# Performance work log

Measured on AMD Instinct MI355X. Metric: run time of the kernel, lower is better.

The kernel has to match this reference:

```python
import jax, jax.numpy as jnp
import numpy as np

BITS = 8
BOUND = 2.0 ** (BITS - 1) - 1.0  # 127, symmetric int8 bound
EPS = 1e-6


def fake_quant(x, scale):
    """Symmetric fake quantization with straight-through estimator."""
    q = jnp.clip(jnp.round(x * scale), -BOUND, BOUND) / scale
    return x + jax.lax.stop_gradient(q - x)


def dense_aqt(x, w, b, mask):
    """AQT-style quantized dense: per-tensor input scale (masked stats),
    per-output-channel weight scale, int8-range fake quant, float GEMM.
    x: [N, Cin], w: [Cin, Cout], b: [Cout], mask: [N, 1]."""
    x_max = jnp.max(jnp.abs(x * mask))                       # masked per-tensor stat
    sx = BOUND / jnp.maximum(x_max, EPS)
    w_max = jnp.max(jnp.abs(w), axis=0, keepdims=True)        # [1, Cout]
    sw = BOUND / jnp.maximum(w_max, EPS)
    xq = fake_quant(x, sx)
    wq = fake_quant(w, sw)
    return jnp.matmul(xq, wq) + b


def setup_inputs() -> dict:
    key = jax.random.key(0)
    k1, k2, k3 = jax.random.split(key, 3)
    B, S, C, H = 4, 2048, 1024, 4096
    inputs = jax.random.normal(k1, (B, S, C), dtype=jnp.float32)
    padding_mask = jnp.ones((B, S, 1), dtype=jnp.float32)
    W1 = jax.random.normal(k2, (C, H), dtype=jnp.float32) * (1.0 / np.sqrt(C))
    b1 = jnp.zeros((H,), dtype=jnp.float32)
    W2 = jax.random.normal(k3, (H, C), dtype=jnp.float32) * (1.0 / np.sqrt(H))
    b2 = jnp.zeros((C,), dtype=jnp.float32)
    return {"inputs": inputs, "padding_mask": padding_mask,
            "W1": W1, "b1": b1, "W2": W2, "b2": b2}


def reference(inputs, padding_mask, W1, b1, W2, b2):
    B, S, C = inputs.shape
    x = inputs.reshape(B * S, C)
    m = padding_mask.reshape(B * S, 1)
    h = jax.nn.relu(dense_aqt(x, W1, b1, m))   # dropout is no-op (deterministic)
    out = dense_aqt(h, W2, b2, m)              # dropout is no-op (deterministic)
    return out.reshape(B, S, C)
```

## Files before the change

### kernel.cpp

```cpp
#include <hip/hip_runtime.h>
#include <hip/hip_fp16.h>
#include <stdint.h>


#define EPSQ 1e-6f
typedef int v4i __attribute__((ext_vector_type(4)));
typedef int v16i __attribute__((ext_vector_type(16)));

__device__ __forceinline__ void async16(const int8_t* g, int8_t* l) {
  __builtin_amdgcn_global_load_lds(
      (const __attribute__((address_space(1))) void*)g,
      (__attribute__((address_space(3))) void*)l, 16, 0, 0);
}
__device__ __forceinline__ unsigned short f2h(float f) {
  __half h = __float2half(f);
  return *(unsigned short*)&h;
}
__device__ __forceinline__ float4 max4(float4 m, float4 v) {
  m.x = fmaxf(m.x, fabsf(v.x)); m.y = fmaxf(m.y, fabsf(v.y));
  m.z = fmaxf(m.z, fabsf(v.z)); m.w = fmaxf(m.w, fabsf(v.w));
  return m;
}
__device__ __forceinline__ unsigned qmb(float x, float s) {
  return __float_as_uint(fmaf(x, s, 12582912.0f)) & 0xffu;
}
__device__ __forceinline__ unsigned q4f(float4 f, float s) {
  return qmb(f.x, s) | (qmb(f.y, s) << 8) | (qmb(f.z, s) << 16) |
         (__float_as_uint(fmaf(f.w, s, 12582912.0f)) << 24);
}
__device__ __forceinline__ unsigned q4h(unsigned ua, unsigned ub,
                                        __half2 s2, __half2 m2) {
  __half2 ha = __hfma2(*(__half2*)&ua, s2, m2);
  __half2 hb = __hfma2(*(__half2*)&ub, s2, m2);
  unsigned va = *(unsigned*)&ha, vb = *(unsigned*)&hb;
#if __has_builtin(__builtin_amdgcn_perm)
  return __builtin_amdgcn_perm(vb, va, 0x06040200u);
#else
  return (va & 0xffu) | ((va >> 8) & 0xff00u) |
         ((vb & 0xffu) << 16) | (((vb >> 8) & 0xff00u) << 16);
#endif
}

__global__ __launch_bounds__(256) void k_stats(
    const float* __restrict__ x, const float* __restrict__ mask,
    const float* __restrict__ W1, const float* __restrict__ W2,
    float* __restrict__ pmaxX, float* __restrict__ pcm1, float* __restrict__ pcm2) {
  const int bx = blockIdx.x, tid = threadIdx.x;
  if (bx < 64) {
    const int sp = bx & 15, cg = bx >> 4;
    const int col = cg * 1024 + tid * 4;
    float4 m = {0.f, 0.f, 0.f, 0.f};
#pragma unroll 8
    for (int r = 0; r < 64; ++r)
      m = max4(m, *(const float4*)(W1 + (size_t)(sp * 64 + r) * 4096 + col));
    *(float4*)(pcm1 + sp * 4096 + col) = m;
  } else if (bx < 128) {
    const int sp = bx - 64;
    const int col = tid * 4;
    float4 m = {0.f, 0.f, 0.f, 0.f};
#pragma unroll 8
    for (int r = 0; r < 64; ++r)
      m = max4(m, *(const float4*)(W2 + (size_t)(sp * 64 + r) * 1024 + col));
    *(float4*)(pcm2 + sp * 1024 + col) = m;
  } else {
    __shared__ float red[4];
    const int b = bx - 128;
    float lmax = 0.f;
    for (int c = b * 256 + tid; c < 1048576; c += 262144) {
      size_t idx = (size_t)c * 8;
      float mk = fabsf(mask[idx >> 10]);
      float4 m4 = {0.f, 0.f, 0.f, 0.f};
      m4 = max4(m4, *(const float4*)(x + idx));
      m4 = max4(m4, *(const float4*)(x + idx + 4));
      lmax = fmaxf(lmax, fmaxf(fmaxf(m4.x, m4.y), fmaxf(m4.z, m4.w)) * mk);
    }
    for (int s = 32; s; s >>= 1) lmax = fmaxf(lmax, __shfl_down(lmax, s));
    if ((tid & 63) == 0) red[tid >> 6] = lmax;
    __syncthreads();
    if (tid == 0)
      pmaxX[b] = fmaxf(fmaxf(red[0], red[1]), fmaxf(red[2], red[3]));
  }
}

__global__ __launch_bounds__(256) void k_quant(
    const float* __restrict__ x, const float* __restrict__ W1, const float* __restrict__ W2,
    const float* __restrict__ pmaxX, const float* __restrict__ pcm1, const float* __restrict__ pcm2,
    int8_t* __restrict__ qx, int8_t* __restrict__ qw1, int8_t* __restrict__ qw2,
    float* __restrict__ cm1, float* __restrict__ cm2, float* __restrict__ scG) {
  const int bx = blockIdx.x, tid = threadIdx.x;
  if (bx < 2048) {
    __shared__ float red[4];
    float v = fmaxf(fmaxf(pmaxX[tid], pmaxX[tid + 256]),
                    fmaxf(pmaxX[tid + 512], pmaxX[tid + 768]));
    for (int s = 32; s; s >>= 1) v = fmaxf(v, __shfl_down(v, s));
    if ((tid & 63) == 0) red[tid >> 6] = v;
    __syncthreads();
    const float xmax = fmaxf(fmaxf(red[0], red[1]), fmaxf(red[2], red[3]));
    if (bx == 0 && tid == 0) scG[0] = xmax;
    const float s = 127.0f / fmaxf(xmax, EPSQ);
    const int wave = tid >> 6, lane = tid & 63;
    const int f = bx * 4 + wave;
    const int r = (f >> 5) * 32 + (lane & 31);
    const int k = (f & 31) * 32 + (lane >> 5) * 16;
    const float4* src = (const float4*)(x + (size_t)r * 1024 + k);
    uint4 o;
    o.x = q4f(src[0], s); o.y = q4f(src[1], s);
    o.z = q4f(src[2], s); o.w = q4f(src[3], s);
    *(uint4*)(qx + (size_t)f * 1024 + lane * 16) = o;
  } else if (bx < 2304) {
    int id = (bx - 2048) * 256 + tid;
    int n4 = id & 1023, kc = id >> 10;
    const int col = n4 * 4;
    float4 cm = {0.f, 0.f, 0.f, 0.f};
#pragma unroll
    for (int sp = 0; sp < 16; ++sp) {
      float4 p = *(const float4*)(pcm1 + sp * 4096 + col);
      cm.x = fmaxf(cm.x, p.x); cm.y = fmaxf(cm.y, p.y);
      cm.z = fmaxf(cm.z, p.z); cm.w = fmaxf(cm.w, p.w);
    }
    if (kc == 0) *(float4*)(cm1 + col) = cm;
    const float s0 = 127.0f / fmaxf(cm.x, EPSQ), s1 = 127.0f / fmaxf(cm.y, EPSQ);
    const float s2 = 127.0f / fmaxf(cm.z, EPSQ), s3 = 127.0f / fmaxf(cm.w, EPSQ);
    union { int8_t p[16]; uint4 v; } u0, u1, u2, u3;
#pragma unroll
    for (int j = 0; j < 16; ++j) {
      float4 f = *(const float4*)(W1 + (size_t)(kc * 16 + j) * 4096 + col);
      u0.p[j] = (int8_t)qmb(f.x, s0); u1.p[j] = (int8_t)qmb(f.y, s1);
      u2.p[j] = (int8_t)qmb(f.z, s2); u3.p[j] = (int8_t)qmb(f.w, s3);
    }
    int8_t* base = qw1 + ((size_t)(col >> 5) * 32 + (kc >> 1)) * 1024 +
                   (kc & 1) * 512 + (col & 31) * 16;
    *(uint4*)(base) = u0.v;      *(uint4*)(base + 16) = u1.v;
    *(uint4*)(base + 32) = u2.v; *(uint4*)(base + 48) = u3.v;
  } else {
    int id = (bx - 2304) * 256 + tid;
    int n4 = id & 255, kc = id >> 8;
    const int col = n4 * 4;
    float4 cm = {0.f, 0.f, 0.f, 0.f};
#pragma unroll
    for (int sp = 0; sp < 64; ++sp) {
      float4 p = *(const float4*)(pcm2 + sp * 1024 + col);
      cm.x = fmaxf(cm.x, p.x); cm.y = fmaxf(cm.y, p.y);
      cm.z = fmaxf(cm.z, p.z); cm.w = fmaxf(cm.w, p.w);
    }
    if (kc == 0) *(float4*)(cm2 + col) = cm;
    const float s0 = 127.0f / fmaxf(cm.x, EPSQ), s1 = 127.0f / fmaxf(cm.y, EPSQ);
    const float s2 = 127.0f / fmaxf(cm.z, EPSQ), s3 = 127.0f / fmaxf(cm.w, EPSQ);
    union { int8_t p[16]; uint4 v; } u0, u1, u2, u3;
#pragma unroll
    for (int j = 0; j < 16; ++j) {
      float4 f = *(const float4*)(W2 + (size_t)(kc * 16 + j) * 1024 + col);
      u0.p[j] = (int8_t)qmb(f.x, s0); u1.p[j] = (int8_t)qmb(f.y, s1);
      u2.p[j] = (int8_t)qmb(f.z, s2); u3.p[j] = (int8_t)qmb(f.w, s3);
    }
    int8_t* base = qw2 + ((size_t)(col >> 5) * 128 + (kc >> 1)) * 1024 +
                   (kc & 1) * 512 + (col & 31) * 16;
    *(uint4*)(base) = u0.v;      *(uint4*)(base + 16) = u1.v;
    *(uint4*)(base + 32) = u2.v; *(uint4*)(base + 48) = u3.v;
  }
}

__global__ __launch_bounds__(512, 6) void gemm1(
    const int8_t* __restrict__ A, const int8_t* __restrict__ Bt,
    const float* __restrict__ sxp, const float* __restrict__ cmax,
    const float* __restrict__ bias, const float* __restrict__ mask,
    unsigned short* __restrict__ hfrag, float* __restrict__ pmaxH) {
  constexpr int NST = 16;
  __shared__ __align__(16) int8_t smem[3 * 16384];
  const int tid = threadIdx.x;
  const int wave = tid >> 6, lane = tid & 63;

  const int bid = blockIdx.x;
  const int xcd = bid & 7, sl = bid >> 3;
  const int m0 = ((xcd & 3) * 16 + (sl & 15)) * 128;
  const int n0 = ((xcd >> 2) * 16 + (sl >> 4)) * 128;
  const int wm = (wave & 1) * 64, wn = (wave >> 1) * 32;

  v16i acc[2] = {};

  const int skc = wave >> 2, sfr = wave & 3;
  const int8_t* gA = A  + ((size_t)((m0 >> 5) + sfr) * 32 + skc) * 1024 + lane * 16;
  const int8_t* gB = Bt + ((size_t)((n0 >> 5) + sfr) * 32 + skc) * 1024 + lane * 16;
  const int soff = (skc * 4 + sfr) * 1024 + lane * 16;

  async16(gA, smem + soff);
  async16(gB, smem + 8192 + soff);
  async16(gA + 2048, smem + 16384 + soff);
  async16(gB + 2048, smem + 16384 + 8192 + soff);
  asm volatile("s_waitcnt vmcnt(2)" ::: "memory");
  __builtin_amdgcn_s_barrier();
  __builtin_amdgcn_sched_barrier(0);

  const int mI = (wave & 1) * 2, nb = wave >> 1;
#pragma unroll
  for (int kb = 0; kb < NST; ++kb) {
    const int co = (kb % 3) * 16384;
    if (kb + 2 < NST) {
      const int po = ((kb + 2) % 3) * 16384;
      async16(gA + (kb + 2) * 2048, smem + po + soff);
      async16(gB + (kb + 2) * 2048, smem + po + 8192 + soff);
    }
    __builtin_amdgcn_sched_barrier(0);
#pragma unroll
    for (int kc = 0; kc < 2; ++kc) {
      v4i af0 = *(const v4i*)(smem + co + (kc * 4 + mI) * 1024 + lane * 16);
      v4i af1 = *(const v4i*)(smem + co + (kc * 4 + mI + 1) * 1024 + lane * 16);
      v4i bf  = *(const v4i*)(smem + co + 8192 + (kc * 4 + nb) * 1024 + lane * 16);
      acc[0] = __builtin_amdgcn_mfma_i32_32x32x32_i8(af0, bf, acc[0], 0, 0, 0);
      acc[1] = __builtin_amdgcn_mfma_i32_32x32x32_i8(af1, bf, acc[1], 0, 0, 0);
    }
    if (kb + 1 < NST) {
      asm volatile("s_waitcnt lgkmcnt(0)" ::: "memory");
      if (kb + 2 < NST)
        asm volatile("s_waitcnt vmcnt(2)" ::: "memory");
      else
        asm volatile("s_waitcnt vmcnt(0)" ::: "memory");
      __builtin_amdgcn_s_barrier();
      __builtin_amdgcn_sched_barrier(0);
    }
  }

  const float asc = fmaxf(sxp[0], EPSQ) * (1.0f / 127.0f);
  const int cl = lane & 31;
  const int rbase = 4 * (lane >> 5);
  const int col = n0 + wn + cl;
  const float bsc = fmaxf(cmax[col], EPSQ) * (1.0f / 127.0f) * asc;
  const float bv = bias[col];
  const int hwoff = (cl >> 4) * 512 + (cl & 15);
  const size_t kblk = (size_t)(n0 + wn) >> 5;
  float lmax = 0.f;
#pragma unroll
  for (int mt = 0; mt < 2; ++mt) {
    const size_t rowblk = (size_t)((m0 + wm + mt * 32) >> 5);
    unsigned short* hb = hfrag + (rowblk * 128 + kblk) * 1024 + hwoff;
    const int rowbase = m0 + wm + mt * 32;
#pragma unroll
    for (int g = 0; g < 4; ++g)
#pragma unroll
      for (int r2 = 0; r2 < 4; ++r2) {
        const int rloc = g * 8 + r2 + rbase;
        const float mk = fabsf(mask[rowbase + rloc]);
        float v = (float)acc[mt][g * 4 + r2] * bsc + bv;
        v = fmaxf(v, 0.f);
        hb[rloc * 16] = f2h(v);
        lmax = fmaxf(lmax, v * mk);
      }
  }
  for (int s = 32; s; s >>= 1) lmax = fmaxf(lmax, __shfl_down(lmax, s));
  __syncthreads();
  float* redf = (float*)smem;
  if (lane == 0) redf[wave] = lmax;
  __syncthreads();
  if (tid == 0) {
    float r = redf[0];
#pragma unroll
    for (int j = 1; j < 8; ++j) r = fmaxf(r, redf[j]);
    pmaxH[bid] = r;
  }
}

__global__ __launch_bounds__(512, 4) void gemm2(
    const unsigned short* __restrict__ hfrag, const int8_t* __restrict__ Bt,
    const float* __restrict__ pmaxH, const float* __restrict__ cmax,
    const float* __restrict__ bias, float* __restrict__ out) {
  constexpr int KF = 2, Kf = 128;
  __shared__ __align__(16) int8_t smem[32768];
  int8_t* const lsA = smem;
  int8_t* const lsB = smem + 16384;
  const int tid = threadIdx.x;
  const int wave = tid >> 6, lane = tid & 63;

  float* red = (float*)smem;
  float v = 0.f;
#pragma unroll
  for (int j = 0; j < 4; ++j) v = fmaxf(v, pmaxH[tid + 512 * j]);
  for (int s = 32; s; s >>= 1) v = fmaxf(v, __shfl_down(v, s));
  if (lane == 0) red[wave] = v;
  __syncthreads();
  float hmax = red[0];
#pragma unroll
  for (int j = 1; j < 8; ++j) hmax = fmaxf(hmax, red[j]);
  __syncthreads();
  const float asc = fmaxf(hmax, EPSQ) * (1.0f / 127.0f);
  const __half sh = __float2half_rn(127.0f / fmaxf(hmax, EPSQ));
  const __half2 s2 = __halves2half2(sh, sh);
  const __half mh = __float2half_rn(1536.0f);
  const __half2 m2 = __halves2half2(mh, mh);

  const int bid = blockIdx.x;
  const int xcd = bid & 7, slot = bid >> 3;
  const int m0 = ((xcd << 3) + (slot >> 3)) * 128;
  const int n0 = (slot & 7) * 128;
  const int wm = (wave & 1) * 64, wn = (wave >> 1) * 32;

  v16i acc[2] = {};

  const int skc = wave >> 2, sfr = wave & 3;
  const uint4* hA = (const uint4*)hfrag;
  const size_t aIdx = ((size_t)((m0 >> 5) + sfr) * Kf + skc) * 128 + lane * 2;
  const int8_t* gB = Bt + ((size_t)((n0 >> 5) + sfr) * Kf + skc) * 1024 + lane * 16;
  int8_t* const dA = lsA + (skc * 4 + sfr) * 1024 + lane * 16;
  int8_t* const dB = lsB + (skc * 4 + sfr) * 1024 + lane * 16;

  const int nsteps = 4096 / (32 * KF);
  const int mI = (wave & 1) * 2, nb = wave >> 1;

  uint4 rA0 = {0, 0, 0, 0}, rB0 = {0, 0, 0, 0};
  uint4 rA1 = {0, 0, 0, 0}, rB1 = {0, 0, 0, 0};

  {
    uint4 a = hA[aIdx], b = hA[aIdx + 1];
    async16(gB, dB);
    __builtin_amdgcn_sched_barrier(0);
    rA1 = hA[aIdx + (size_t)(KF * 128)];
    rB1 = hA[aIdx + (size_t)(KF * 128) + 1];
    uint4 o;
    o.x = q4h(a.x, a.y, s2, m2); o.y = q4h(a.z, a.w, s2, m2);
    o.z = q4h(b.x, b.y, s2, m2); o.w = q4h(b.z, b.w, s2, m2);
    *(uint4*)dA = o;
  }
  asm volatile("s_waitcnt lgkmcnt(0)" ::: "memory");
  asm volatile("s_waitcnt vmcnt(2)" ::: "memory");
  __builtin_amdgcn_s_barrier();
  __builtin_amdgcn_sched_barrier(0);

#pragma unroll 2
  for (int kb = 0; kb < nsteps; ++kb) {
    const int cur = kb & 1;
    const int co = cur * 8192, po = co ^ 8192;
    const bool more = (kb + 1 < nsteps);
    const bool deep = (kb + 2 < nsteps);
    if (more) {
      async16(gB + (size_t)(kb + 1) * (KF * 1024), dB + po);
      __builtin_amdgcn_sched_barrier(0);
      if (deep) {
        const size_t ai = aIdx + (size_t)(kb + 2) * (KF * 128);
        if (cur) { rA1 = hA[ai]; rB1 = hA[ai + 1]; }
        else     { rA0 = hA[ai]; rB0 = hA[ai + 1]; }
      }
    }
#pragma unroll
    for (int kc = 0; kc < KF; ++kc) {
      v4i af0 = *(const v4i*)(lsA + co + (kc * 4 + mI) * 1024 + lane * 16);
      v4i af1 = *(const v4i*)(lsA + co + (kc * 4 + mI + 1) * 1024 + lane * 16);
      v4i bf  = *(const v4i*)(lsB + co + (kc * 4 + nb) * 1024 + lane * 16);
      acc[0] = __builtin_amdgcn_mfma_i32_32x32x32_i8(af0, bf, acc[0], 0, 0, 0);
      acc[1] = __builtin_amdgcn_mfma_i32_32x32x32_i8(af1, bf, acc[1], 0, 0, 0);
    }
    if (more) {
      const uint4 pa = cur ? rA0 : rA1;
      const uint4 pb = cur ? rB0 : rB1;
      uint4 o;
      o.x = q4h(pa.x, pa.y, s2, m2); o.y = q4h(pa.z, pa.w, s2, m2);
      o.z = q4h(pb.x, pb.y, s2, m2); o.w = q4h(pb.z, pb.w, s2, m2);
      *(uint4*)(dA + po) = o;
      asm volatile("s_waitcnt lgkmcnt(0)" ::: "memory");
      if (deep) asm volatile("s_waitcnt vmcnt(2)" ::: "memory");
      else      asm volatile("s_waitcnt vmcnt(0)" ::: "memory");
      __builtin_amdgcn_s_barrier();
      __builtin_amdgcn_sched_barrier(0);
    }
  }

  const int cl = lane & 31;
  const int rbase = 4 * (lane >> 5);
  const int col = n0 + wn + cl;
  const float bsc = fmaxf(cmax[col], EPSQ) * (1.0f / 127.0f) * asc;
  const float bv = bias[col];
#pragma unroll
  for (int mt = 0; mt < 2; ++mt)
#pragma unroll
    for (int g = 0; g < 4; ++g)
#pragma unroll
      for (int r2 = 0; r2 < 4; ++r2) {
        const int row = m0 + wm + mt * 32 + g * 8 + r2 + rbase;
        out[(size_t)row * 1024 + col] = (float)acc[mt][g * 4 + r2] * bsc + bv;
      }
}

extern "C" void kernel_launch(void* const* d_in, const int* in_sizes, int n_in,
                              void* d_out, int out_size, void* d_ws, size_t ws_size,
                              hipStream_t stream) {
  const float* x  = (const float*)d_in[0];
  const float* mk = (const float*)d_in[1];
  const float* W1 = (const float*)d_in[2];
  const float* b1 = (const float*)d_in[3];
  const float* W2 = (const float*)d_in[4];
  const float* b2 = (const float*)d_in[5];
  float* out = (float*)d_out;

  float* scG   = (float*)d_ws;
  float* pmaxX = scG + 8;
  float* pmaxH = pmaxX + 1024;
  float* pcm1  = pmaxH + 2048;
  float* pcm2  = pcm1 + 65536;
  float* cm1   = pcm2 + 65536;
  float* cm2   = cm1 + 4096;
  int8_t* qx  = (int8_t*)(cm2 + 1024);
  int8_t* qw1 = qx  + (size_t)8192 * 1024;
  int8_t* qw2 = qw1 + (size_t)4096 * 1024;
  unsigned short* h = (unsigned short*)(qw2 + (size_t)1024 * 4096);

  k_stats<<<1152, 256, 0, stream>>>(x, mk, W1, W2, pmaxX, pcm1, pcm2);
  k_quant<<<2560, 256, 0, stream>>>(x, W1, W2, pmaxX, pcm1, pcm2,
                                    qx, qw1, qw2, cm1, cm2, scG);
  gemm1<<<2048, 512, 0, stream>>>(qx, qw1, scG, cm1, b1, mk, h, pmaxH);
  gemm2<<<512, 512, 0, stream>>>(h, qw2, pmaxH, cm2, b2, out);
}
```

Measured before the change: 223.1 us.

## Give each wave a 2x2 MFMA tile and enlarge gemm1 block tile

gemm1 now computes a 256x128 tile per block (1024 blocks), with each wave holding a 2x2 grid of 32x32 accumulators, so every A and B fragment read from LDS feeds two MFMAs. gemm2 drops to 256 threads per block, with each wave also computing a 2x2 accumulator tile and loading two k-fragments of A and B per thread. The aim is more MFMA work per LDS read and per global load. The cost is more registers and LDS per block, lower occupancy (launch bounds 4 and 2), and fewer waves to hide latency.

```diff
diff --git a/kernel.cpp b/kernel.cpp
--- a/kernel.cpp
+++ b/kernel.cpp
@@ -160,59 +160,66 @@
   }
 }
 
-__global__ __launch_bounds__(512, 6) void gemm1(
+__global__ __launch_bounds__(512, 4) void gemm1(
     const int8_t* __restrict__ A, const int8_t* __restrict__ Bt,
     const float* __restrict__ sxp, const float* __restrict__ cmax,
     const float* __restrict__ bias, const float* __restrict__ mask,
     unsigned short* __restrict__ hfrag, float* __restrict__ pmaxH) {
   constexpr int NST = 16;
-  __shared__ __align__(16) int8_t smem[3 * 16384];
+  constexpr int BUF = 24576;
+  __shared__ __align__(16) int8_t smem[3 * BUF];
   const int tid = threadIdx.x;
   const int wave = tid >> 6, lane = tid & 63;
 
   const int bid = blockIdx.x;
   const int xcd = bid & 7, sl = bid >> 3;
-  const int m0 = ((xcd & 3) * 16 + (sl & 15)) * 128;
-  const int n0 = ((xcd >> 2) * 16 + (sl >> 4)) * 128;
-  const int wm = (wave & 1) * 64, wn = (wave >> 1) * 32;
-
-  v16i acc[2] = {};
-
-  const int skc = wave >> 2, sfr = wave & 3;
-  const int8_t* gA = A  + ((size_t)((m0 >> 5) + sfr) * 32 + skc) * 1024 + lane * 16;
-  const int8_t* gB = Bt + ((size_t)((n0 >> 5) + sfr) * 32 + skc) * 1024 + lane * 16;
-  const int soff = (skc * 4 + sfr) * 1024 + lane * 16;
-
-  async16(gA, smem + soff);
-  async16(gB, smem + 8192 + soff);
-  async16(gA + 2048, smem + 16384 + soff);
-  async16(gB + 2048, smem + 16384 + 8192 + soff);
-  asm volatile("s_waitcnt vmcnt(2)" ::: "memory");
+  const int m0 = (xcd * 4 + (sl & 3)) * 256;
+  const int n0 = (sl >> 2) * 128;
+
+  v16i acc[2][2] = {};
+
+  const int8_t* gA = A  + ((size_t)((m0 >> 5) + wave) * 32) * 1024 + lane * 16;
+  const int8_t* gB = Bt + ((size_t)((n0 >> 5) + (wave & 3)) * 32 + (wave >> 2)) * 1024
+                     + lane * 16;
+  const int dAo = wave * 1024 + lane * 16;
+  const int dBo = 16384 + ((wave >> 2) * 4 + (wave & 3)) * 1024 + lane * 16;
+
+  async16(gA,        smem + dAo);
+  async16(gA + 1024, smem + dAo + 8192);
+  async16(gB,        smem + dBo);
+  async16(gA + 2048, smem + BUF + dAo);
+  async16(gA + 3072, smem + BUF + dAo + 8192);
+  async16(gB + 2048, smem + BUF + dBo);
+  asm volatile("s_waitcnt vmcnt(3)" ::: "memory");
   __builtin_amdgcn_s_barrier();
   __builtin_amdgcn_sched_barrier(0);
 
-  const int mI = (wave & 1) * 2, nb = wave >> 1;
+  const int mI = (wave & 3) * 2, nI = (wave >> 2) * 2;
 #pragma unroll
   for (int kb = 0; kb < NST; ++kb) {
-    const int co = (kb % 3) * 16384;
+    const int co = (kb % 3) * BUF;
     if (kb + 2 < NST) {
-      const int po = ((kb + 2) % 3) * 16384;
-      async16(gA + (kb + 2) * 2048, smem + po + soff);
-      async16(gB + (kb + 2) * 2048, smem + po + 8192 + soff);
+      const int po = ((kb + 2) % 3) * BUF;
+      async16(gA + (kb + 2) * 2048,        smem + po + dAo);
+      async16(gA + (kb + 2) * 2048 + 1024, smem + po + dAo + 8192);
+      async16(gB + (kb + 2) * 2048,        smem + po + dBo);
     }
     __builtin_amdgcn_sched_barrier(0);
 #pragma unroll
     for (int kc = 0; kc < 2; ++kc) {
-      v4i af0 = *(const v4i*)(smem + co + (kc * 4 + mI) * 1024 + lane * 16);
-      v4i af1 = *(const v4i*)(smem + co + (kc * 4 + mI + 1) * 1024 + lane * 16);
-      v4i bf  = *(const v4i*)(smem + co + 8192 + (kc * 4 + nb) * 1024 + lane * 16);
-      acc[0] = __builtin_amdgcn_mfma_i32_32x32x32_i8(af0, bf, acc[0], 0, 0, 0);
-      acc[1] = __builtin_amdgcn_mfma_i32_32x32x32_i8(af1, bf, acc[1], 0, 0, 0);
+      v4i af0 = *(const v4i*)(smem + co + (kc * 8 + mI) * 1024 + lane * 16);
+      v4i af1 = *(const v4i*)(smem + co + (kc * 8 + mI + 1) * 1024 + lane * 16);
+      v4i bf0 = *(const v4i*)(smem + co + 16384 + (kc * 4 + nI) * 1024 + lane * 16);
+      v4i bf1 = *(const v4i*)(smem + co + 16384 + (kc * 4 + nI + 1) * 1024 + lane * 16);
+      acc[0][0] = __builtin_amdgcn_mfma_i32_32x32x32_i8(af0, bf0, acc[0][0], 0, 0, 0);
+      acc[0][1] = __builtin_amdgcn_mfma_i32_32x32x32_i8(af0, bf1, acc[0][1], 0, 0, 0);
+      acc[1][0] = __builtin_amdgcn_mfma_i32_32x32x32_i8(af1, bf0, acc[1][0], 0, 0, 0);
+      acc[1][1] = __builtin_amdgcn_mfma_i32_32x32x32_i8(af1, bf1, acc[1][1], 0, 0, 0);
     }
     if (kb + 1 < NST) {
       asm volatile("s_waitcnt lgkmcnt(0)" ::: "memory");
       if (kb + 2 < NST)
-        asm volatile("s_waitcnt vmcnt(2)" ::: "memory");
+        asm volatile("s_waitcnt vmcnt(3)" ::: "memory");
       else
         asm volatile("s_waitcnt vmcnt(0)" ::: "memory");
       __builtin_amdgcn_s_barrier();
@@ -223,27 +230,34 @@
   const float asc = fmaxf(sxp[0], EPSQ) * (1.0f / 127.0f);
   const int cl = lane & 31;
   const int rbase = 4 * (lane >> 5);
-  const int col = n0 + wn + cl;
-  const float bsc = fmaxf(cmax[col], EPSQ) * (1.0f / 127.0f) * asc;
-  const float bv = bias[col];
+  const int wr = wave & 3, wc = wave >> 2;
+  float bsc[2], bv[2];
+#pragma unroll
+  for (int nt = 0; nt < 2; ++nt) {
+    const int col = n0 + wc * 64 + nt * 32 + cl;
+    bsc[nt] = fmaxf(cmax[col], EPSQ) * (1.0f / 127.0f) * asc;
+    bv[nt] = bias[col];
+  }
   const int hwoff = (cl >> 4) * 512 + (cl & 15);
-  const size_t kblk = (size_t)(n0 + wn) >> 5;
   float lmax = 0.f;
 #pragma unroll
   for (int mt = 0; mt < 2; ++mt) {
-    const size_t rowblk = (size_t)((m0 + wm + mt * 32) >> 5);
-    unsigned short* hb = hfrag + (rowblk * 128 + kblk) * 1024 + hwoff;
-    const int rowbase = m0 + wm + mt * 32;
+    const int rowbase = m0 + wr * 64 + mt * 32;
+    const size_t rowblk = (size_t)(rowbase >> 5);
 #pragma unroll
     for (int g = 0; g < 4; ++g)
 #pragma unroll
       for (int r2 = 0; r2 < 4; ++r2) {
         const int rloc = g * 8 + r2 + rbase;
         const float mk = fabsf(mask[rowbase + rloc]);
-        float v = (float)acc[mt][g * 4 + r2] * bsc + bv;
-        v = fmaxf(v, 0.f);
-        hb[rloc * 16] = f2h(v);
-        lmax = fmaxf(lmax, v * mk);
+#pragma unroll
+        for (int nt = 0; nt < 2; ++nt) {
+          const size_t kblk = (size_t)((n0 + wc * 64 + nt * 32) >> 5);
+          float v = (float)acc[mt][nt][g * 4 + r2] * bsc[nt] + bv[nt];
+          v = fmaxf(v, 0.f);
+          hfrag[(rowblk * 128 + kblk) * 1024 + hwoff + rloc * 16] = f2h(v);
+          lmax = fmaxf(lmax, v * mk);
+        }
       }
   }
   for (int s = 32; s; s >>= 1) lmax = fmaxf(lmax, __shfl_down(lmax, s));
@@ -259,11 +273,10 @@
   }
 }
 
-__global__ __launch_bounds__(512, 4) void gemm2(
+__global__ __launch_bounds__(256, 2) void gemm2(
     const unsigned short* __restrict__ hfrag, const int8_t* __restrict__ Bt,
     const float* __restrict__ pmaxH, const float* __restrict__ cmax,
     const float* __restrict__ bias, float* __restrict__ out) {
-  constexpr int KF = 2, Kf = 128;
   __shared__ __align__(16) int8_t smem[32768];
   int8_t* const lsA = smem;
   int8_t* const lsB = smem + 16384;
@@ -273,13 +286,11 @@
   float* red = (float*)smem;
   float v = 0.f;
 #pragma unroll
-  for (int j = 0; j < 4; ++j) v = fmaxf(v, pmaxH[tid + 512 * j]);
+  for (int j = 0; j < 4; ++j) v = fmaxf(v, pmaxH[tid + 256 * j]);
   for (int s = 32; s; s >>= 1) v = fmaxf(v, __shfl_down(v, s));
   if (lane == 0) red[wave] = v;
   __syncthreads();
-  float hmax = red[0];
-#pragma unroll
-  for (int j = 1; j < 8; ++j) hmax = fmaxf(hmax, red[j]);
+  const float hmax = fmaxf(fmaxf(red[0], red[1]), fmaxf(red[2], red[3]));
   __syncthreads();
   const float asc = fmaxf(hmax, EPSQ) * (1.0f / 127.0f);
   const __half sh = __float2half_rn(127.0f / fmaxf(hmax, EPSQ));
@@ -291,36 +302,41 @@
   const int xcd = bid & 7, slot = bid >> 3;
   const int m0 = ((xcd << 3) + (slot >> 3)) * 128;
   const int n0 = (slot & 7) * 128;
-  const int wm = (wave & 1) * 64, wn = (wave >> 1) * 32;
-
-  v16i acc[2] = {};
-
-  const int skc = wave >> 2, sfr = wave & 3;
+
+  v16i acc[2][2] = {};
+
   const uint4* hA = (const uint4*)hfrag;
-  const size_t aIdx = ((size_t)((m0 >> 5) + sfr) * Kf + skc) * 128 + lane * 2;
-  const int8_t* gB = Bt + ((size_t)((n0 >> 5) + sfr) * Kf + skc) * 1024 + lane * 16;
-  int8_t* const dA = lsA + (skc * 4 + sfr) * 1024 + lane * 16;
-  int8_t* const dB = lsB + (skc * 4 + sfr) * 1024 + lane * 16;
-
-  const int nsteps = 4096 / (32 * KF);
-  const int mI = (wave & 1) * 2, nb = wave >> 1;
-
-  uint4 rA0 = {0, 0, 0, 0}, rB0 = {0, 0, 0, 0};
-  uint4 rA1 = {0, 0, 0, 0}, rB1 = {0, 0, 0, 0};
+  const size_t aBase = ((size_t)((m0 >> 5) + wave) * 128) * 128 + lane * 2;
+  const int8_t* gB = Bt + ((size_t)((n0 >> 5) + wave) * 128) * 1024 + lane * 16;
+  int8_t* const dA0 = lsA + (0 * 4 + wave) * 1024 + lane * 16;
+  int8_t* const dA1 = lsA + (1 * 4 + wave) * 1024 + lane * 16;
+  int8_t* const dB0 = lsB + (0 * 4 + wave) * 1024 + lane * 16;
+  int8_t* const dB1 = lsB + (1 * 4 + wave) * 1024 + lane * 16;
+
+  const int nsteps = 64;
+  const int mI = (wave & 1) * 2, nI = (wave >> 1) * 2;
+
+  uint4 s0a0 = {}, s0a1 = {}, s0c0 = {}, s0c1 = {};
+  uint4 s1a0 = {}, s1a1 = {}, s1c0 = {}, s1c1 = {};
 
   {
-    uint4 a = hA[aIdx], b = hA[aIdx + 1];
-    async16(gB, dB);
+    uint4 a0 = hA[aBase], a1 = hA[aBase + 1];
+    uint4 c0 = hA[aBase + 128], c1 = hA[aBase + 129];
+    async16(gB, dB0);
+    async16(gB + 1024, dB1);
     __builtin_amdgcn_sched_barrier(0);
-    rA1 = hA[aIdx + (size_t)(KF * 128)];
-    rB1 = hA[aIdx + (size_t)(KF * 128) + 1];
+    s1a0 = hA[aBase + 2 * 128]; s1a1 = hA[aBase + 2 * 128 + 1];
+    s1c0 = hA[aBase + 3 * 128]; s1c1 = hA[aBase + 3 * 128 + 1];
     uint4 o;
-    o.x = q4h(a.x, a.y, s2, m2); o.y = q4h(a.z, a.w, s2, m2);
-    o.z = q4h(b.x, b.y, s2, m2); o.w = q4h(b.z, b.w, s2, m2);
-    *(uint4*)dA = o;
+    o.x = q4h(a0.x, a0.y, s2, m2); o.y = q4h(a0.z, a0.w, s2, m2);
+    o.z = q4h(a1.x, a1.y, s2, m2); o.w = q4h(a1.z, a1.w, s2, m2);
+    *(uint4*)dA0 = o;
+    o.x = q4h(c0.x, c0.y, s2, m2); o.y = q4h(c0.z, c0.w, s2, m2);
+    o.z = q4h(c1.x, c1.y, s2, m2); o.w = q4h(c1.z, c1.w, s2, m2);
+    *(uint4*)dA1 = o;
   }
   asm volatile("s_waitcnt lgkmcnt(0)" ::: "memory");
-  asm volatile("s_waitcnt vmcnt(2)" ::: "memory");
+  asm volatile("s_waitcnt vmcnt(4)" ::: "memory");
   __builtin_amdgcn_s_barrier();
   __builtin_amdgcn_sched_barrier(0);
 
@@ -331,31 +347,40 @@
     const bool more = (kb + 1 < nsteps);
     const bool deep = (kb + 2 < nsteps);
     if (more) {
-      async16(gB + (size_t)(kb + 1) * (KF * 1024), dB + po);
+      async16(gB + (size_t)((kb + 1) * 2) * 1024, dB0 + po);
+      async16(gB + (size_t)((kb + 1) * 2 + 1) * 1024, dB1 + po);
       __builtin_amdgcn_sched_barrier(0);
       if (deep) {
-        const size_t ai = aIdx + (size_t)(kb + 2) * (KF * 128);
-        if (cur) { rA1 = hA[ai]; rB1 = hA[ai + 1]; }
-        else     { rA0 = hA[ai]; rB0 = hA[ai + 1]; }
+        const size_t ai = aBase + (size_t)((kb + 2) * 2) * 128;
+        if (cur) { s1a0 = hA[ai]; s1a1 = hA[ai + 1];
+                   s1c0 = hA[ai + 128]; s1c1 = hA[ai + 129]; }
+        else     { s0a0 = hA[ai]; s0a1 = hA[ai + 1];
+                   s0c0 = hA[ai + 128]; s0c1 = hA[ai + 129]; }
       }
     }
 #pragma unroll
-    for (int kc = 0; kc < KF; ++kc) {
+    for (int kc = 0; kc < 2; ++kc) {
       v4i af0 = *(const v4i*)(lsA + co + (kc * 4 + mI) * 1024 + lane * 16);
       v4i af1 = *(const v4i*)(lsA + co + (kc * 4 + mI + 1) * 1024 + lane * 16);
-      v4i bf  = *(const v4i*)(lsB + co + (kc * 4 + nb) * 1024 + lane * 16);
-      acc[0] = __builtin_amdgcn_mfma_i32_32x32x32_i8(af0, bf, acc[0], 0, 0, 0);
-      acc[1] = __builtin_amdgcn_mfma_i32_32x32x32_i8(af1, bf, acc[1], 0, 0, 0);
+      v4i bf0 = *(const v4i*)(lsB + co + (kc * 4 + nI) * 1024 + lane * 16);
+      v4i bf1 = *(const v4i*)(lsB + co + (kc * 4 + nI + 1) * 1024 + lane * 16);
+      acc[0][0] = __builtin_amdgcn_mfma_i32_32x32x32_i8(af0, bf0, acc[0][0], 0, 0, 0);
+      acc[0][1] = __builtin_amdgcn_mfma_i32_32x32x32_i8(af0, bf1, acc[0][1], 0, 0, 0);
+      acc[1][0] = __builtin_amdgcn_mfma_i32_32x32x32_i8(af1, bf0, acc[1][0], 0, 0, 0);
+      acc[1][1] = __builtin_amdgcn_mfma_i32_32x32x32_i8(af1, bf1, acc[1][1], 0, 0, 0);
     }
     if (more) {
-      const uint4 pa = cur ? rA0 : rA1;
-      const uint4 pb = cur ? rB0 : rB1;
+      const uint4 pa0 = cur ? s0a0 : s1a0, pa1 = cur ? s0a1 : s1a1;
+      const uint4 pc0 = cur ? s0c0 : s1c0, pc1 = cur ? s0c1 : s1c1;
       uint4 o;
-      o.x = q4h(pa.x, pa.y, s2, m2); o.y = q4h(pa.z, pa.w, s2, m2);
-      o.z = q4h(pb.x, pb.y, s2, m2); o.w = q4h(pb.z, pb.w, s2, m2);
-      *(uint4*)(dA + po) = o;
+      o.x = q4h(pa0.x, pa0.y, s2, m2); o.y = q4h(pa0.z, pa0.w, s2, m2);
+      o.z = q4h(pa1.x, pa1.y, s2, m2); o.w = q4h(pa1.z, pa1.w, s2, m2);
+      *(uint4*)(dA0 + po) = o;
+      o.x = q4h(pc0.x, pc0.y, s2, m2); o.y = q4h(pc0.z, pc0.w, s2, m2);
+      o.z = q4h(pc1.x, pc1.y, s2, m2); o.w = q4h(pc1.z, pc1.w, s2, m2);
+      *(uint4*)(dA1 + po) = o;
       asm volatile("s_waitcnt lgkmcnt(0)" ::: "memory");
-      if (deep) asm volatile("s_waitcnt vmcnt(2)" ::: "memory");
+      if (deep) asm volatile("s_waitcnt vmcnt(4)" ::: "memory");
       else      asm volatile("s_waitcnt vmcnt(0)" ::: "memory");
       __builtin_amdgcn_s_barrier();
       __builtin_amdgcn_sched_barrier(0);
@@ -364,17 +389,26 @@
 
   const int cl = lane & 31;
   const int rbase = 4 * (lane >> 5);
-  const int col = n0 + wn + cl;
-  const float bsc = fmaxf(cmax[col], EPSQ) * (1.0f / 127.0f) * asc;
-  const float bv = bias[col];
+  const int wr = wave & 1, wc = wave >> 1;
+  float bsc[2], bv[2];
+  int colv[2];
+#pragma unroll
+  for (int nt = 0; nt < 2; ++nt) {
+    colv[nt] = n0 + wc * 64 + nt * 32 + cl;
+    bsc[nt] = fmaxf(cmax[colv[nt]], EPSQ) * (1.0f / 127.0f) * asc;
+    bv[nt] = bias[colv[nt]];
+  }
 #pragma unroll
   for (int mt = 0; mt < 2; ++mt)
 #pragma unroll
     for (int g = 0; g < 4; ++g)
 #pragma unroll
       for (int r2 = 0; r2 < 4; ++r2) {
-        const int row = m0 + wm + mt * 32 + g * 8 + r2 + rbase;
-        out[(size_t)row * 1024 + col] = (float)acc[mt][g * 4 + r2] * bsc + bv;
+        const int row = m0 + wr * 64 + mt * 32 + g * 8 + r2 + rbase;
+#pragma unroll
+        for (int nt = 0; nt < 2; ++nt)
+          out[(size_t)row * 1024 + colv[nt]] =
+              (float)acc[mt][nt][g * 4 + r2] * bsc[nt] + bv[nt];
       }
 }
 
@@ -404,6 +438,6 @@
   k_stats<<<1152, 256, 0, stream>>>(x, mk, W1, W2, pmaxX, pcm1, pcm2);
   k_quant<<<2560, 256, 0, stream>>>(x, W1, W2, pmaxX, pcm1, pcm2,
                                     qx, qw1, qw2, cm1, cm2, scG);
-  gemm1<<<2048, 512, 0, stream>>>(qx, qw1, scG, cm1, b1, mk, h, pmaxH);
-  gemm2<<<512, 512, 0, stream>>>(h, qw2, pmaxH, cm2, b2, out);
-}
+  gemm1<<<1024, 512, 0, stream>>>(qx, qw1, scG, cm1, b1, mk, h, pmaxH);
+  gemm2<<<512, 256, 0, stream>>>(h, qw2, pmaxH, cm2, b2, out);
+}
```

Result: slower. 228.0 us (+2.2%).
